# Optimization experiments

Measured on AMD Instinct MI355X. Metric: run time of the kernel, lower is better.

## Reference

```python
import jax, jax.numpy as jnp
import numpy as np


def setup_inputs() -> dict:
    key = jax.random.key(0)
    k1, k2 = jax.random.split(key)
    b, t, f = 64, 2048, 1024
    hidden_decoder = jax.random.normal(k1, (b, f), dtype=jnp.float32)
    hiddens_encoder = jax.random.normal(k2, (b, t, f), dtype=jnp.float32)
    return {"hidden_decoder": hidden_decoder, "hiddens_encoder": hiddens_encoder}


def reference(hidden_decoder, hiddens_encoder):
    # scores[b, t] = <hidden_decoder[b], hiddens_encoder[b, t]>
    # (the original loops over t, computes full bxb matmuls and takes diagonals;
    #  this is the equivalent batched dot product)
    scores = jnp.einsum("bf,btf->bt", hidden_decoder, hiddens_encoder)
    a = jax.nn.softmax(scores, axis=1)  # (b, t)
    # context[b, f] = sum_t a[b, t] * hiddens_encoder[b, t, f]
    context = jnp.einsum("bt,btf->bf", a, hiddens_encoder)
    return context
```

## Files before the change

### kernel.cpp

```cpp
#include <hip/hip_runtime.h>
#include <math.h>


#define BB 64
#define TT 2048
#define FF 1024
#define RR 4

typedef __attribute__((address_space(1))) const void* gas_ptr;
typedef __attribute__((address_space(3))) void* las_ptr;

__device__ __forceinline__ void gld_lds16(const float* g, float* l) {
    __builtin_amdgcn_global_load_lds((gas_ptr)g, (las_ptr)l, 16, 0, 0);
}

__global__ __launch_bounds__(256) void attn_pass1(
    const float* __restrict__ hd, const float* __restrict__ he,
    float* __restrict__ part_ctx, float* __restrict__ part_m,
    float* __restrict__ part_l, int S, int Tc)
{
    const int bid  = blockIdx.x;
    const int b    = bid / S;
    const int s    = bid - b * S;
    const int t0   = s * Tc;
    const int lane = threadIdx.x & 63;
    const int wave = threadIdx.x >> 6;
    const int nt   = Tc / RR;

    __shared__ float buf[2][RR * FF];

    const float* hdb = hd + (size_t)b * FF;
    float4 hdv[4];
#pragma unroll
    for (int k = 0; k < 4; ++k)
        hdv[k] = *(const float4*)(hdb + 4 * lane + 256 * k);

    const float* heb = he + ((size_t)b * TT + t0) * (size_t)FF;

    float m = -INFINITY, l = 0.f;
    float4 ctx = make_float4(0.f, 0.f, 0.f, 0.f);

    {
        const float* row = heb + (size_t)wave * FF;
#pragma unroll
        for (int k = 0; k < 4; ++k)
            gld_lds16(row + k * 256 + lane * 4, &buf[0][wave * FF + k * 256]);
    }

    for (int kt = 0; kt < nt; ++kt) {
        const int cur = kt & 1;
        __syncthreads();

        if (kt + 1 < nt) {
            const float* row = heb + ((size_t)(kt + 1) * RR + wave) * FF;
#pragma unroll
            for (int k = 0; k < 4; ++k)
                gld_lds16(row + k * 256 + lane * 4,
                          &buf[cur ^ 1][wave * FF + k * 256]);
        }

        float d[RR];
#pragma unroll
        for (int r = 0; r < RR; ++r) {
            float4 hv[4];
#pragma unroll
            for (int k = 0; k < 4; ++k)
                hv[k] = *(const float4*)&buf[cur][r * FF + 4 * lane + 256 * k];
            float acc = 0.f;
#pragma unroll
            for (int k = 0; k < 4; ++k)
                acc += hdv[k].x * hv[k].x + hdv[k].y * hv[k].y +
                       hdv[k].z * hv[k].z + hdv[k].w * hv[k].w;
            d[r] = acc;
        }
#pragma unroll
        for (int off = 32; off >= 1; off >>= 1) {
#pragma unroll
            for (int r = 0; r < RR; ++r)
                d[r] += __shfl_xor(d[r], off, 64);
        }

        float mn = m;
#pragma unroll
        for (int r = 0; r < RR; ++r) mn = fmaxf(mn, d[r]);
        const float alpha = __expf(m - mn);
        float w[RR], wsum = 0.f;
#pragma unroll
        for (int r = 0; r < RR; ++r) { w[r] = __expf(d[r] - mn); wsum += w[r]; }

        const int f4 = threadIdx.x * 4;
        float4 a = make_float4(ctx.x * alpha, ctx.y * alpha,
                               ctx.z * alpha, ctx.w * alpha);
#pragma unroll
        for (int r = 0; r < RR; ++r) {
            const float4 rv = *(const float4*)&buf[cur][r * FF + f4];
            a.x += w[r] * rv.x; a.y += w[r] * rv.y;
            a.z += w[r] * rv.z; a.w += w[r] * rv.w;
        }
        ctx = a;
        l = l * alpha + wsum;
        m = mn;
    }

    *(float4*)(part_ctx + (size_t)bid * FF + threadIdx.x * 4) = ctx;
    if (threadIdx.x == 0) { part_m[bid] = m; part_l[bid] = l; }
}

__global__ __launch_bounds__(256) void attn_pass2(
    const float* __restrict__ part_ctx, const float* __restrict__ part_m,
    const float* __restrict__ part_l, float* __restrict__ out, int S)
{
    const int b = blockIdx.x;

    float M = -INFINITY;
    for (int s = 0; s < S; ++s) M = fmaxf(M, part_m[b * S + s]);
    float L = 0.f;
    for (int s = 0; s < S; ++s)
        L += part_l[b * S + s] * __expf(part_m[b * S + s] - M);

    const int f4 = threadIdx.x * 4;
    float4 acc = make_float4(0.f, 0.f, 0.f, 0.f);
    for (int s = 0; s < S; ++s) {
        const float e  = __expf(part_m[b * S + s] - M);
        const float4 c = *(const float4*)(part_ctx + ((size_t)(b * S + s)) * FF + f4);
        acc.x += e * c.x; acc.y += e * c.y; acc.z += e * c.z; acc.w += e * c.w;
    }
    const float inv = 1.f / L;
    float4 o = make_float4(acc.x * inv, acc.y * inv, acc.z * inv, acc.w * inv);
    *(float4*)(out + (size_t)b * FF + f4) = o;
}

extern "C" void kernel_launch(void* const* d_in, const int* in_sizes, int n_in,
                              void* d_out, int out_size, void* d_ws, size_t ws_size,
                              hipStream_t stream) {
    const float* hd = (const float*)d_in[0];
    const float* he = (const float*)d_in[1];
    float* out = (float*)d_out;

    int S = 32;
    while (S > 1 && (size_t)BB * S * (FF * sizeof(float) + 2 * sizeof(float)) > ws_size)
        S >>= 1;
    const int Tc = TT / S;

    float* part_ctx = (float*)d_ws;
    float* part_m   = part_ctx + (size_t)BB * S * FF;
    float* part_l   = part_m + (size_t)BB * S;

    attn_pass1<<<BB * S, 256, 0, stream>>>(hd, he, part_ctx, part_m, part_l, S, Tc);
    attn_pass2<<<BB, 256, 0, stream>>>(part_ctx, part_m, part_l, out, S);
}
```

Measured before the change: 696.3 us.

## Triple-buffer LDS staging with vmcnt waits and per-wave score computation

Moves pass1 from double to triple buffering of encoder rows in LDS, prefetching two tiles ahead. Before each barrier it waits on vmcnt for only the oldest tile, so more loads stay in flight. Each wave now computes the dot product for its own row instead of all four rows, cutting redundant LDS reads and shuffles. The scores are shared through LDS, which adds a second barrier per iteration. Pass2 is split across 4x more blocks of 64 threads to raise parallelism in the combine step.

```diff
diff --git a/kernel.cpp b/kernel.cpp
--- a/kernel.cpp
+++ b/kernel.cpp
@@ -6,12 +6,20 @@
 #define TT 2048
 #define FF 1024
 #define RR 4
+#define NBUF 3
 
 typedef __attribute__((address_space(1))) const void* gas_ptr;
 typedef __attribute__((address_space(3))) void* las_ptr;
 
 __device__ __forceinline__ void gld_lds16(const float* g, float* l) {
     __builtin_amdgcn_global_load_lds((gas_ptr)g, (las_ptr)l, 16, 0, 0);
+}
+
+__device__ __forceinline__ void stage_row(const float* __restrict__ row,
+                                          float* dst, int lane) {
+#pragma unroll
+    for (int k = 0; k < 4; ++k)
+        gld_lds16(row + k * 256 + lane * 4, dst + k * 256);
 }
 
 __global__ __launch_bounds__(256) void attn_pass1(
@@ -27,7 +35,8 @@
     const int wave = threadIdx.x >> 6;
     const int nt   = Tc / RR;
 
-    __shared__ float buf[2][RR * FF];
+    __shared__ __align__(16) float buf[NBUF][RR * FF];
+    __shared__ __align__(16) float scores[RR];
 
     const float* hdb = hd + (size_t)b * FF;
     float4 hdv[4];
@@ -40,65 +49,63 @@
     float m = -INFINITY, l = 0.f;
     float4 ctx = make_float4(0.f, 0.f, 0.f, 0.f);
 
-    {
-        const float* row = heb + (size_t)wave * FF;
-#pragma unroll
-        for (int k = 0; k < 4; ++k)
-            gld_lds16(row + k * 256 + lane * 4, &buf[0][wave * FF + k * 256]);
-    }
+    stage_row(heb + (size_t)wave * FF, &buf[0][wave * FF], lane);
+    stage_row(heb + (size_t)(RR + wave) * FF, &buf[1][wave * FF], lane);
 
     for (int kt = 0; kt < nt; ++kt) {
-        const int cur = kt & 1;
-        __syncthreads();
+        const int cur = kt % NBUF;
 
         if (kt + 1 < nt) {
-            const float* row = heb + ((size_t)(kt + 1) * RR + wave) * FF;
-#pragma unroll
-            for (int k = 0; k < 4; ++k)
-                gld_lds16(row + k * 256 + lane * 4,
-                          &buf[cur ^ 1][wave * FF + k * 256]);
+            asm volatile("s_waitcnt vmcnt(4)" ::: "memory");
+        } else {
+            asm volatile("s_waitcnt vmcnt(0)" ::: "memory");
         }
+        __builtin_amdgcn_sched_barrier(0);
+        __builtin_amdgcn_s_barrier();
+        __builtin_amdgcn_sched_barrier(0);
 
-        float d[RR];
-#pragma unroll
-        for (int r = 0; r < RR; ++r) {
+        if (kt + 2 < nt)
+            stage_row(heb + ((size_t)(kt + 2) * RR + wave) * FF,
+                      &buf[(kt + 2) % NBUF][wave * FF], lane);
+
+        {
+            const float* rp = &buf[cur][wave * FF];
             float4 hv[4];
 #pragma unroll
             for (int k = 0; k < 4; ++k)
-                hv[k] = *(const float4*)&buf[cur][r * FF + 4 * lane + 256 * k];
+                hv[k] = *(const float4*)(rp + 4 * lane + 256 * k);
             float acc = 0.f;
 #pragma unroll
             for (int k = 0; k < 4; ++k)
                 acc += hdv[k].x * hv[k].x + hdv[k].y * hv[k].y +
                        hdv[k].z * hv[k].z + hdv[k].w * hv[k].w;
-            d[r] = acc;
-        }
 #pragma unroll
-        for (int off = 32; off >= 1; off >>= 1) {
-#pragma unroll
-            for (int r = 0; r < RR; ++r)
-                d[r] += __shfl_xor(d[r], off, 64);
+            for (int off = 32; off >= 1; off >>= 1)
+                acc += __shfl_xor(acc, off, 64);
+            if (lane == 0) scores[wave] = acc;
         }
 
-        float mn = m;
-#pragma unroll
-        for (int r = 0; r < RR; ++r) mn = fmaxf(mn, d[r]);
+        asm volatile("s_waitcnt lgkmcnt(0)" ::: "memory");
+        __builtin_amdgcn_sched_barrier(0);
+        __builtin_amdgcn_s_barrier();
+        __builtin_amdgcn_sched_barrier(0);
+
+        const float4 sc = *(const float4*)scores;
+        float mn = fmaxf(fmaxf(m, fmaxf(sc.x, sc.y)), fmaxf(sc.z, sc.w));
         const float alpha = __expf(m - mn);
-        float w[RR], wsum = 0.f;
-#pragma unroll
-        for (int r = 0; r < RR; ++r) { w[r] = __expf(d[r] - mn); wsum += w[r]; }
+        const float w0 = __expf(sc.x - mn), w1 = __expf(sc.y - mn);
+        const float w2 = __expf(sc.z - mn), w3 = __expf(sc.w - mn);
 
         const int f4 = threadIdx.x * 4;
-        float4 a = make_float4(ctx.x * alpha, ctx.y * alpha,
-                               ctx.z * alpha, ctx.w * alpha);
-#pragma unroll
-        for (int r = 0; r < RR; ++r) {
-            const float4 rv = *(const float4*)&buf[cur][r * FF + f4];
-            a.x += w[r] * rv.x; a.y += w[r] * rv.y;
-            a.z += w[r] * rv.z; a.w += w[r] * rv.w;
-        }
-        ctx = a;
-        l = l * alpha + wsum;
+        const float4 r0 = *(const float4*)&buf[cur][0 * FF + f4];
+        const float4 r1 = *(const float4*)&buf[cur][1 * FF + f4];
+        const float4 r2 = *(const float4*)&buf[cur][2 * FF + f4];
+        const float4 r3 = *(const float4*)&buf[cur][3 * FF + f4];
+        ctx.x = ctx.x * alpha + w0 * r0.x + w1 * r1.x + w2 * r2.x + w3 * r3.x;
+        ctx.y = ctx.y * alpha + w0 * r0.y + w1 * r1.y + w2 * r2.y + w3 * r3.y;
+        ctx.z = ctx.z * alpha + w0 * r0.z + w1 * r1.z + w2 * r2.z + w3 * r3.z;
+        ctx.w = ctx.w * alpha + w0 * r0.w + w1 * r1.w + w2 * r2.w + w3 * r3.w;
+        l = l * alpha + (w0 + w1 + w2 + w3);
         m = mn;
     }
 
@@ -106,11 +113,12 @@
     if (threadIdx.x == 0) { part_m[bid] = m; part_l[bid] = l; }
 }
 
-__global__ __launch_bounds__(256) void attn_pass2(
+__global__ __launch_bounds__(64) void attn_pass2(
     const float* __restrict__ part_ctx, const float* __restrict__ part_m,
     const float* __restrict__ part_l, float* __restrict__ out, int S)
 {
-    const int b = blockIdx.x;
+    const int b  = blockIdx.x >> 2;
+    const int f4 = ((blockIdx.x & 3) * 64 + threadIdx.x) * 4;
 
     float M = -INFINITY;
     for (int s = 0; s < S; ++s) M = fmaxf(M, part_m[b * S + s]);
@@ -118,7 +126,6 @@
     for (int s = 0; s < S; ++s)
         L += part_l[b * S + s] * __expf(part_m[b * S + s] - M);
 
-    const int f4 = threadIdx.x * 4;
     float4 acc = make_float4(0.f, 0.f, 0.f, 0.f);
     for (int s = 0; s < S; ++s) {
         const float e  = __expf(part_m[b * S + s] - M);
@@ -126,8 +133,8 @@
         acc.x += e * c.x; acc.y += e * c.y; acc.z += e * c.z; acc.w += e * c.w;
     }
     const float inv = 1.f / L;
-    float4 o = make_float4(acc.x * inv, acc.y * inv, acc.z * inv, acc.w * inv);
-    *(float4*)(out + (size_t)b * FF + f4) = o;
+    *(float4*)(out + (size_t)b * FF + f4) =
+        make_float4(acc.x * inv, acc.y * inv, acc.z * inv, acc.w * inv);
 }
 
 extern "C" void kernel_launch(void* const* d_in, const int* in_sizes, int n_in,
@@ -147,5 +154,5 @@
     float* part_l   = part_m + (size_t)BB * S;
 
     attn_pass1<<<BB * S, 256, 0, stream>>>(hd, he, part_ctx, part_m, part_l, S, Tc);
-    attn_pass2<<<BB, 256, 0, stream>>>(part_ctx, part_m, part_l, out, S);
+    attn_pass2<<<BB * 4, 64, 0, stream>>>(part_ctx, part_m, part_l, out, S);
 }
```

Result: no change. 698.1 us (+0.3%).
